# Kernel tuning notes

Measured on AMD Instinct MI355X. Metric: run time of the kernel, lower is better.

The kernel has to match this reference:

```python
import jax, jax.numpy as jnp
import numpy as np

T, B, I, H = 1024, 64, 512, 1024

def setup_inputs() -> dict:
    key = jax.random.key(0)
    ks = jax.random.split(key, 7)
    s = 1.0 / np.sqrt(H)
    return {
        "x": jax.random.normal(ks[0], (T, B, I), dtype=jnp.float32),
        "h0": jax.random.normal(ks[1], (B, H), dtype=jnp.float32),
        "c0": jax.random.normal(ks[2], (B, H), dtype=jnp.float32),
        "w_ih": jax.random.normal(ks[3], (4 * H, I), dtype=jnp.float32) * s,
        "w_hh": jax.random.normal(ks[4], (4 * H, H), dtype=jnp.float32) * s,
        "b_ih": jax.random.normal(ks[5], (4 * H,), dtype=jnp.float32) * s,
        "b_hh": jax.random.normal(ks[6], (4 * H,), dtype=jnp.float32) * s,
    }

def reference(x, h0, c0, w_ih, w_hh, b_ih, b_hh):
    # Precompute input projections for all timesteps: [T, B, 4H]
    x_proj = jnp.einsum('tbi,gi->tbg', x, w_ih) + b_ih + b_hh

    def step(carry, xp):
        h, c = carry
        gates = xp + h @ w_hh.T  # [B, 4H]
        i_g, f_g, g_g, o_g = jnp.split(gates, 4, axis=-1)
        i_g = jax.nn.sigmoid(i_g)
        f_g = jax.nn.sigmoid(f_g)
        g_g = jnp.tanh(g_g)
        o_g = jax.nn.sigmoid(o_g)
        c = f_g * c + i_g * g_g
        h = o_g * jnp.tanh(c)
        return (h, c), h

    (h_f, c_f), outputs = jax.lax.scan(step, (h0, c0), x_proj)
    return outputs, (h_f, c_f)
```

## Files before the change

### kernel.cpp

```cpp
#include <hip/hip_runtime.h>

typedef __attribute__((ext_vector_type(8))) short short8;
typedef __attribute__((ext_vector_type(4))) float f32x4;
typedef __attribute__((ext_vector_type(4))) unsigned short u16x4;

#define T_TOT 1024
#define NBATCH 64
#define NIN 512
#define NHID 1024
#define NG 4096
#define BH 65536
#define OUT_MAIN 67108864ull

__device__ __forceinline__ unsigned short f2bf(float f) {
  unsigned int u = __builtin_bit_cast(unsigned int, f);
  u += 0x7fffu + ((u >> 16) & 1u);
  return (unsigned short)(u >> 16);
}
__device__ __forceinline__ float sigf(float x) { return 1.0f / (1.0f + __expf(-x)); }
__device__ __forceinline__ float tanh_f(float x) { return 1.0f - 2.0f / (1.0f + __expf(2.0f * x)); }

__device__ __forceinline__ short8 ldg_coh16(const unsigned short* p) {
  short8 r;
  asm volatile("global_load_dwordx4 %0, %1, off sc0 sc1"
               : "=v"(r) : "v"(p) : "memory");
  return r;
}
__device__ __forceinline__ void stg_coh8(unsigned short* p, u16x4 v) {
  asm volatile("global_store_dwordx2 %0, %1, off sc0 sc1"
               :: "v"(p), "v"(v) : "memory");
}

__global__ void __launch_bounds__(256) prep_kernel(
    const float* __restrict__ w_ih, const float* __restrict__ w_hh,
    const float* __restrict__ b_ih, const float* __restrict__ b_hh,
    const float* __restrict__ h0, const float* __restrict__ c0,
    unsigned short* __restrict__ w_ihb, unsigned short* __restrict__ w_hhb,
    float* __restrict__ bsum, unsigned short* __restrict__ h_state,
    float* __restrict__ c_ws, unsigned int* __restrict__ bar)
{
  int tid = blockIdx.x * blockDim.x + threadIdx.x;
  int stride = gridDim.x * blockDim.x;
  if (tid == 0) *bar = 0u;
  for (int i = tid; i < NG * NHID; i += stride) w_hhb[i] = f2bf(w_hh[i]);
  for (int i = tid; i < NG * NIN; i += stride) w_ihb[i] = f2bf(w_ih[i]);
  for (int i = tid; i < NG; i += stride) bsum[i] = b_ih[i] + b_hh[i];
  for (int i = tid; i < BH; i += stride) { h_state[i] = f2bf(h0[i]); c_ws[i] = c0[i]; }
}

__global__ void __launch_bounds__(256) xp_gemm(
    const float* __restrict__ x,
    const unsigned short* __restrict__ w_ihb,
    float* __restrict__ xp)
{
  __shared__ unsigned short As[128][72];
  __shared__ unsigned short Bs[128][72];
  const int tid = threadIdx.x;
  const int lane = tid & 63;
  const int wave = tid >> 6;
  const int l15 = lane & 15, l4 = lane >> 4;
  const int wy = wave >> 1, wx = wave & 1;
  const int row0 = blockIdx.x * 128;
  const int col0 = blockIdx.y * 128;

  f32x4 acc[4][4];
#pragma unroll
  for (int mt = 0; mt < 4; ++mt)
#pragma unroll
    for (int nt = 0; nt < 4; ++nt) acc[mt][nt] = (f32x4){0.f, 0.f, 0.f, 0.f};

  for (int kb = 0; kb < 8; ++kb) {
    const int k0 = kb * 64;
#pragma unroll
    for (int i = 0; i < 4; ++i) {
      int idx = tid + 256 * i;
      int r = idx >> 3, kc = (idx & 7) * 8;
      const float* src = x + (size_t)(row0 + r) * NIN + k0 + kc;
      float4 f0 = *(const float4*)src;
      float4 f1 = *(const float4*)(src + 4);
      short8 v;
      v[0] = (short)f2bf(f0.x); v[1] = (short)f2bf(f0.y);
      v[2] = (short)f2bf(f0.z); v[3] = (short)f2bf(f0.w);
      v[4] = (short)f2bf(f1.x); v[5] = (short)f2bf(f1.y);
      v[6] = (short)f2bf(f1.z); v[7] = (short)f2bf(f1.w);
      *(short8*)&As[r][kc] = v;
    }
#pragma unroll
    for (int i = 0; i < 4; ++i) {
      int idx = tid + 256 * i;
      int r = idx >> 3, kc = (idx & 7) * 8;
      short8 v = *(const short8*)(w_ihb + (size_t)(col0 + r) * NIN + k0 + kc);
      *(short8*)&Bs[r][kc] = v;
    }
    __syncthreads();
#pragma unroll
    for (int kk = 0; kk < 2; ++kk) {
      const int kl = kk * 32 + l4 * 8;
      short8 a[4], b[4];
#pragma unroll
      for (int mt = 0; mt < 4; ++mt) a[mt] = *(const short8*)&As[wy * 64 + mt * 16 + l15][kl];
#pragma unroll
      for (int nt = 0; nt < 4; ++nt) b[nt] = *(const short8*)&Bs[wx * 64 + nt * 16 + l15][kl];
#pragma unroll
      for (int mt = 0; mt < 4; ++mt)
#pragma unroll
        for (int nt = 0; nt < 4; ++nt)
          acc[mt][nt] = __builtin_amdgcn_mfma_f32_16x16x32_bf16(a[mt], b[nt], acc[mt][nt], 0, 0, 0);
    }
    __syncthreads();
  }
#pragma unroll
  for (int mt = 0; mt < 4; ++mt)
#pragma unroll
    for (int nt = 0; nt < 4; ++nt)
#pragma unroll
      for (int j = 0; j < 4; ++j) {
        int r = row0 + wy * 64 + mt * 16 + l4 * 4 + j;
        int c = col0 + wx * 64 + nt * 16 + l15;
        xp[(size_t)r * NG + c] = acc[mt][nt][j];
      }
}

__device__ __forceinline__ void gbar_nf(unsigned int* bar, unsigned int target) {
  asm volatile("s_waitcnt vmcnt(0)" ::: "memory");
  __syncthreads();
  if (threadIdx.x == 0) {
    __hip_atomic_fetch_add(bar, 1u, __ATOMIC_RELAXED, __HIP_MEMORY_SCOPE_AGENT);
    while (__hip_atomic_load(bar, __ATOMIC_RELAXED, __HIP_MEMORY_SCOPE_AGENT) < target) {
      __builtin_amdgcn_s_sleep(1);
    }
  }
  __syncthreads();
}

__global__ void __launch_bounds__(256, 1) lstm_rec(
    const float* __restrict__ xp,
    const unsigned short* __restrict__ w_hhb,
    const float* __restrict__ bsum,
    unsigned short* __restrict__ h_state,
    float* __restrict__ c_ws,
    float* __restrict__ out,
    unsigned int* __restrict__ bar,
    int t0, int Tc)
{
  __shared__ float part[4][64][68];
  const int tid = threadIdx.x;
  const int lane = tid & 63;
  const int wave = tid >> 6;
  const int l15 = lane & 15;
  const int l4 = lane >> 4;
  const int col0 = blockIdx.x * 16;

  const int er = tid >> 2;
  const int ec = (tid & 3) * 4;

  f32x4 c_reg = *(const f32x4*)&c_ws[er * NHID + col0 + ec];
  f32x4 bias[4];
#pragma unroll
  for (int q = 0; q < 4; ++q) bias[q] = *(const f32x4*)&bsum[q * NHID + col0 + ec];

  short8 breg[4][8];
#pragma unroll
  for (int q = 0; q < 4; ++q)
#pragma unroll
    for (int kk = 0; kk < 8; ++kk) {
      const unsigned short* p =
          w_hhb + (size_t)(q * NHID + col0 + l15) * NHID + wave * 256 + kk * 32 + l4 * 8;
      breg[q][kk] = *(const short8*)p;
    }

  for (int tt = 0; tt < Tc; ++tt) {
    const int t = t0 + tt;
    const unsigned short* h = h_state + (size_t)(t & 1) * BH;
    const unsigned short* hbase = h + (size_t)l15 * NHID + wave * 256 + l4 * 8;

    f32x4 xv[4];
#pragma unroll
    for (int q = 0; q < 4; ++q)
      xv[q] = *(const f32x4*)(xp + ((size_t)tt * NBATCH + er) * NG + q * NHID + col0 + ec);

    f32x4 acc[4][4];
#pragma unroll
    for (int mt = 0; mt < 4; ++mt)
#pragma unroll
      for (int q = 0; q < 4; ++q) acc[mt][q] = (f32x4){0.f, 0.f, 0.f, 0.f};

    short8 abuf[3][4];
#pragma unroll
    for (int mt = 0; mt < 4; ++mt)
      abuf[0][mt] = ldg_coh16(hbase + mt * 16 * NHID);
#pragma unroll
    for (int mt = 0; mt < 4; ++mt)
      abuf[1][mt] = ldg_coh16(hbase + mt * 16 * NHID + 32);

#pragma unroll
    for (int kk = 0; kk < 8; ++kk) {
      if (kk < 6) {
#pragma unroll
        for (int mt = 0; mt < 4; ++mt)
          abuf[(kk + 2) % 3][mt] = ldg_coh16(hbase + mt * 16 * NHID + (kk + 2) * 32);
        asm volatile("s_waitcnt vmcnt(8)" ::: "memory");
      } else if (kk == 6) {
        asm volatile("s_waitcnt vmcnt(4)" ::: "memory");
      } else {
        asm volatile("s_waitcnt vmcnt(0)" ::: "memory");
      }
      __builtin_amdgcn_sched_barrier(0);
#pragma unroll
      for (int mt = 0; mt < 4; ++mt)
#pragma unroll
        for (int q = 0; q < 4; ++q)
          acc[mt][q] = __builtin_amdgcn_mfma_f32_16x16x32_bf16(
              abuf[kk % 3][mt], breg[q][kk], acc[mt][q], 0, 0, 0);
    }

#pragma unroll
    for (int mt = 0; mt < 4; ++mt)
#pragma unroll
      for (int q = 0; q < 4; ++q)
#pragma unroll
        for (int j = 0; j < 4; ++j)
          part[wave][mt * 16 + l4 * 4 + j][q * 16 + l15] = acc[mt][q][j];
    __syncthreads();

    f32x4 g[4];
#pragma unroll
    for (int q = 0; q < 4; ++q) {
      f32x4 s = *(const f32x4*)&part[0][er][q * 16 + ec];
      s += *(const f32x4*)&part[1][er][q * 16 + ec];
      s += *(const f32x4*)&part[2][er][q * 16 + ec];
      s += *(const f32x4*)&part[3][er][q * 16 + ec];
      g[q] = s + bias[q] + xv[q];
    }
    f32x4 hv4;
    u16x4 hb4;
#pragma unroll
    for (int j = 0; j < 4; ++j) {
      float ig = sigf(g[0][j]);
      float fg = sigf(g[1][j]);
      float gg = tanh_f(g[2][j]);
      float og = sigf(g[3][j]);
      float c = fg * c_reg[j] + ig * gg;
      c_reg[j] = c;
      float hv = og * tanh_f(c);
      hv4[j] = hv;
      hb4[j] = f2bf(hv);
    }
    *(f32x4*)&out[(size_t)t * BH + (size_t)er * NHID + col0 + ec] = hv4;
    stg_coh8(h_state + (size_t)((t + 1) & 1) * BH + er * NHID + col0 + ec, hb4);
    if (t == T_TOT - 1) {
      *(f32x4*)&out[OUT_MAIN + (size_t)er * NHID + col0 + ec] = hv4;
      *(f32x4*)&out[OUT_MAIN + BH + (size_t)er * NHID + col0 + ec] = c_reg;
    }

    gbar_nf(bar, (unsigned int)(t + 1) * 64u);
  }

  *(f32x4*)&c_ws[er * NHID + col0 + ec] = c_reg;
}

extern "C" void kernel_launch(void* const* d_in, const int* in_sizes, int n_in,
                              void* d_out, int out_size, void* d_ws, size_t ws_size,
                              hipStream_t stream) {
  const float* x   = (const float*)d_in[0];
  const float* h0  = (const float*)d_in[1];
  const float* c0  = (const float*)d_in[2];
  const float* wih = (const float*)d_in[3];
  const float* whh = (const float*)d_in[4];
  const float* bih = (const float*)d_in[5];
  const float* bhh = (const float*)d_in[6];
  float* out = (float*)d_out;

  char* base = (char*)d_ws;
  size_t off = 0;
  auto alloc = [&](size_t bytes) {
    char* r = base + off;
    off += (bytes + 255) & ~(size_t)255;
    return r;
  };
  unsigned short* w_hhb   = (unsigned short*)alloc((size_t)NG * NHID * 2);
  unsigned short* w_ihb   = (unsigned short*)alloc((size_t)NG * NIN * 2);
  float*          bsum    = (float*)alloc((size_t)NG * 4);
  unsigned short* h_state = (unsigned short*)alloc(2ull * BH * 2);
  float*          c_ws    = (float*)alloc((size_t)BH * 4);
  unsigned int*   bar     = (unsigned int*)alloc(256);

  int Tc = T_TOT;
  while (Tc > 2 && off + (size_t)Tc * NBATCH * NG * 4 > ws_size) Tc >>= 1;
  float* xp = (float*)alloc((size_t)Tc * NBATCH * NG * 4);

  prep_kernel<<<dim3(512), dim3(256), 0, stream>>>(
      wih, whh, bih, bhh, h0, c0, w_ihb, w_hhb, bsum, h_state, c_ws, bar);

  for (int t0 = 0; t0 < T_TOT; t0 += Tc) {
    xp_gemm<<<dim3(Tc / 2, 32), dim3(256), 0, stream>>>(
        x + (size_t)t0 * NBATCH * NIN, w_ihb, xp);
    lstm_rec<<<dim3(64), dim3(256), 0, stream>>>(
        xp, w_hhb, bsum, h_state, c_ws, out, bar, t0, Tc);
  }
}
```

Measured before the change: 9.880 ms.

## Replace global atomic barrier with per-wave flags and issue all h loads upfront

Replaces the per-timestep global atomic-counter barrier with per-wave flag words. Each wave publishes its timestep after storing its h slice, and consumers poll all 256 flags with one coherent load per lane before reading h. The h loads for all eight k-groups are now issued together using immediate offsets, followed by staged waitcnts, instead of a three-deep rolling buffer. The out store moves after the flag publish to take it off the critical path. This adds a __syncthreads between the partial-sum read and the next step's overwrite, and costs extra registers for the larger load buffer.

Result: faster. 8.872 ms (-10.2%).

```diff
diff --git a/kernel.cpp b/kernel.cpp
--- a/kernel.cpp
+++ b/kernel.cpp
@@ -20,15 +20,25 @@
 __device__ __forceinline__ float sigf(float x) { return 1.0f / (1.0f + __expf(-x)); }
 __device__ __forceinline__ float tanh_f(float x) { return 1.0f - 2.0f / (1.0f + __expf(2.0f * x)); }
 
-__device__ __forceinline__ short8 ldg_coh16(const unsigned short* p) {
+template<int OFS>
+__device__ __forceinline__ short8 ldg_coh16_o(const unsigned short* p) {
   short8 r;
-  asm volatile("global_load_dwordx4 %0, %1, off sc0 sc1"
-               : "=v"(r) : "v"(p) : "memory");
+  asm volatile("global_load_dwordx4 %0, %1, off offset:%2 sc0 sc1"
+               : "=v"(r) : "v"(p), "i"(OFS) : "memory");
   return r;
 }
 __device__ __forceinline__ void stg_coh8(unsigned short* p, u16x4 v) {
   asm volatile("global_store_dwordx2 %0, %1, off sc0 sc1"
                :: "v"(p), "v"(v) : "memory");
+}
+__device__ __forceinline__ unsigned int ld_coh32(const unsigned int* p) {
+  unsigned int r;
+  asm volatile("global_load_dword %0, %1, off sc0 sc1\n\ts_waitcnt vmcnt(0)"
+               : "=v"(r) : "v"(p) : "memory");
+  return r;
+}
+__device__ __forceinline__ void st_coh32(unsigned int* p, unsigned int v) {
+  asm volatile("global_store_dword %0, %1, off sc0 sc1" :: "v"(p), "v"(v) : "memory");
 }
 
 __global__ void __launch_bounds__(256) prep_kernel(
@@ -37,11 +47,11 @@
     const float* __restrict__ h0, const float* __restrict__ c0,
     unsigned short* __restrict__ w_ihb, unsigned short* __restrict__ w_hhb,
     float* __restrict__ bsum, unsigned short* __restrict__ h_state,
-    float* __restrict__ c_ws, unsigned int* __restrict__ bar)
+    float* __restrict__ c_ws, unsigned int* __restrict__ flags)
 {
   int tid = blockIdx.x * blockDim.x + threadIdx.x;
   int stride = gridDim.x * blockDim.x;
-  if (tid == 0) *bar = 0u;
+  for (int i = tid; i < 256; i += stride) flags[i] = 0u;
   for (int i = tid; i < NG * NHID; i += stride) w_hhb[i] = f2bf(w_hh[i]);
   for (int i = tid; i < NG * NIN; i += stride) w_ihb[i] = f2bf(w_ih[i]);
   for (int i = tid; i < NG; i += stride) bsum[i] = b_ih[i] + b_hh[i];
@@ -121,16 +131,26 @@
       }
 }
 
-__device__ __forceinline__ void gbar_nf(unsigned int* bar, unsigned int target) {
-  asm volatile("s_waitcnt vmcnt(0)" ::: "memory");
-  __syncthreads();
-  if (threadIdx.x == 0) {
-    __hip_atomic_fetch_add(bar, 1u, __ATOMIC_RELAXED, __HIP_MEMORY_SCOPE_AGENT);
-    while (__hip_atomic_load(bar, __ATOMIC_RELAXED, __HIP_MEMORY_SCOPE_AGENT) < target) {
-      __builtin_amdgcn_s_sleep(1);
-    }
-  }
-  __syncthreads();
+template<int KK>
+__device__ __forceinline__ void loadk(short8 (&abuf)[8][4],
+    const unsigned short* hb0, const unsigned short* hb1,
+    const unsigned short* hb2, const unsigned short* hb3) {
+  abuf[KK][0] = ldg_coh16_o<KK * 64>(hb0);
+  abuf[KK][1] = ldg_coh16_o<KK * 64>(hb1);
+  abuf[KK][2] = ldg_coh16_o<KK * 64>(hb2);
+  abuf[KK][3] = ldg_coh16_o<KK * 64>(hb3);
+}
+template<int KK>
+__device__ __forceinline__ void kgroup(short8 (&abuf)[8][4],
+    const short8 (&breg)[4][8], f32x4 (&acc)[4][4]) {
+  asm volatile("s_waitcnt vmcnt(%0)" :: "i"(28 - 4 * KK) : "memory");
+  __builtin_amdgcn_sched_barrier(0);
+#pragma unroll
+  for (int mt = 0; mt < 4; ++mt)
+#pragma unroll
+    for (int q = 0; q < 4; ++q)
+      acc[mt][q] = __builtin_amdgcn_mfma_f32_16x16x32_bf16(
+          abuf[KK][mt], breg[q][KK], acc[mt][q], 0, 0, 0);
 }
 
 __global__ void __launch_bounds__(256, 1) lstm_rec(
@@ -140,7 +160,7 @@
     unsigned short* __restrict__ h_state,
     float* __restrict__ c_ws,
     float* __restrict__ out,
-    unsigned int* __restrict__ bar,
+    unsigned int* __restrict__ flags,
     int t0, int Tc)
 {
   __shared__ float part[4][64][68];
@@ -154,6 +174,9 @@
   const int er = tid >> 2;
   const int ec = (tid & 3) * 4;
 
+  unsigned int* myflag = flags + (blockIdx.x * 4 + wave);
+  const unsigned int* pflag = flags + ((wave * 16 + (lane >> 2)) * 4 + (lane & 3));
+
   f32x4 c_reg = *(const f32x4*)&c_ws[er * NHID + col0 + ec];
   f32x4 bias[4];
 #pragma unroll
@@ -173,46 +196,46 @@
     const int t = t0 + tt;
     const unsigned short* h = h_state + (size_t)(t & 1) * BH;
     const unsigned short* hbase = h + (size_t)l15 * NHID + wave * 256 + l4 * 8;
+    const unsigned short* hb0 = hbase;
+    const unsigned short* hb1 = hbase + 16 * NHID;
+    const unsigned short* hb2 = hbase + 32 * NHID;
+    const unsigned short* hb3 = hbase + 48 * NHID;
 
     f32x4 xv[4];
 #pragma unroll
     for (int q = 0; q < 4; ++q)
       xv[q] = *(const f32x4*)(xp + ((size_t)tt * NBATCH + er) * NG + q * NHID + col0 + ec);
 
+    for (;;) {
+      unsigned int v = ld_coh32(pflag);
+      if (__all((int)(v >= (unsigned int)t))) break;
+      __builtin_amdgcn_s_sleep(1);
+    }
+
     f32x4 acc[4][4];
 #pragma unroll
     for (int mt = 0; mt < 4; ++mt)
 #pragma unroll
       for (int q = 0; q < 4; ++q) acc[mt][q] = (f32x4){0.f, 0.f, 0.f, 0.f};
 
-    short8 abuf[3][4];
-#pragma unroll
-    for (int mt = 0; mt < 4; ++mt)
-      abuf[0][mt] = ldg_coh16(hbase + mt * 16 * NHID);
-#pragma unroll
-    for (int mt = 0; mt < 4; ++mt)
-      abuf[1][mt] = ldg_coh16(hbase + mt * 16 * NHID + 32);
-
-#pragma unroll
-    for (int kk = 0; kk < 8; ++kk) {
-      if (kk < 6) {
-#pragma unroll
-        for (int mt = 0; mt < 4; ++mt)
-          abuf[(kk + 2) % 3][mt] = ldg_coh16(hbase + mt * 16 * NHID + (kk + 2) * 32);
-        asm volatile("s_waitcnt vmcnt(8)" ::: "memory");
-      } else if (kk == 6) {
-        asm volatile("s_waitcnt vmcnt(4)" ::: "memory");
-      } else {
-        asm volatile("s_waitcnt vmcnt(0)" ::: "memory");
-      }
-      __builtin_amdgcn_sched_barrier(0);
-#pragma unroll
-      for (int mt = 0; mt < 4; ++mt)
-#pragma unroll
-        for (int q = 0; q < 4; ++q)
-          acc[mt][q] = __builtin_amdgcn_mfma_f32_16x16x32_bf16(
-              abuf[kk % 3][mt], breg[q][kk], acc[mt][q], 0, 0, 0);
-    }
+    short8 abuf[8][4];
+    loadk<0>(abuf, hb0, hb1, hb2, hb3);
+    loadk<1>(abuf, hb0, hb1, hb2, hb3);
+    loadk<2>(abuf, hb0, hb1, hb2, hb3);
+    loadk<3>(abuf, hb0, hb1, hb2, hb3);
+    loadk<4>(abuf, hb0, hb1, hb2, hb3);
+    loadk<5>(abuf, hb0, hb1, hb2, hb3);
+    loadk<6>(abuf, hb0, hb1, hb2, hb3);
+    loadk<7>(abuf, hb0, hb1, hb2, hb3);
+
+    kgroup<0>(abuf, breg, acc);
+    kgroup<1>(abuf, breg, acc);
+    kgroup<2>(abuf, breg, acc);
+    kgroup<3>(abuf, breg, acc);
+    kgroup<4>(abuf, breg, acc);
+    kgroup<5>(abuf, breg, acc);
+    kgroup<6>(abuf, breg, acc);
+    kgroup<7>(abuf, breg, acc);
 
 #pragma unroll
     for (int mt = 0; mt < 4; ++mt)
@@ -232,6 +255,8 @@
       s += *(const f32x4*)&part[3][er][q * 16 + ec];
       g[q] = s + bias[q] + xv[q];
     }
+    __syncthreads();
+
     f32x4 hv4;
     u16x4 hb4;
 #pragma unroll
@@ -246,14 +271,15 @@
       hv4[j] = hv;
       hb4[j] = f2bf(hv);
     }
+    stg_coh8(h_state + (size_t)((t + 1) & 1) * BH + er * NHID + col0 + ec, hb4);
+    asm volatile("s_waitcnt vmcnt(0)" ::: "memory");
+    if (lane == 0) st_coh32(myflag, (unsigned int)(t + 1));
+
     *(f32x4*)&out[(size_t)t * BH + (size_t)er * NHID + col0 + ec] = hv4;
-    stg_coh8(h_state + (size_t)((t + 1) & 1) * BH + er * NHID + col0 + ec, hb4);
     if (t == T_TOT - 1) {
       *(f32x4*)&out[OUT_MAIN + (size_t)er * NHID + col0 + ec] = hv4;
       *(f32x4*)&out[OUT_MAIN + BH + (size_t)er * NHID + col0 + ec] = c_reg;
     }
-
-    gbar_nf(bar, (unsigned int)(t + 1) * 64u);
   }
 
   *(f32x4*)&c_ws[er * NHID + col0 + ec] = c_reg;
@@ -283,19 +309,19 @@
   float*          bsum    = (float*)alloc((size_t)NG * 4);
   unsigned short* h_state = (unsigned short*)alloc(2ull * BH * 2);
   float*          c_ws    = (float*)alloc((size_t)BH * 4);
-  unsigned int*   bar     = (unsigned int*)alloc(256);
+  unsigned int*   flags   = (unsigned int*)alloc(1024);
 
   int Tc = T_TOT;
   while (Tc > 2 && off + (size_t)Tc * NBATCH * NG * 4 > ws_size) Tc >>= 1;
   float* xp = (float*)alloc((size_t)Tc * NBATCH * NG * 4);
 
   prep_kernel<<<dim3(512), dim3(256), 0, stream>>>(
-      wih, whh, bih, bhh, h0, c0, w_ihb, w_hhb, bsum, h_state, c_ws, bar);
+      wih, whh, bih, bhh, h0, c0, w_ihb, w_hhb, bsum, h_state, c_ws, flags);
 
   for (int t0 = 0; t0 < T_TOT; t0 += Tc) {
     xp_gemm<<<dim3(Tc / 2, 32), dim3(256), 0, stream>>>(
         x + (size_t)t0 * NBATCH * NIN, w_ihb, xp);
     lstm_rec<<<dim3(64), dim3(256), 0, stream>>>(
-        xp, w_hhb, bsum, h_state, c_ws, out, bar, t0, Tc);
+        xp, w_hhb, bsum, h_state, c_ws, out, flags, t0, Tc);
   }
 }
```
